# Optimization experiments

Hardware: AMD Instinct MI355X
Metric: run time of the kernel (lower is better)

## Reference

```python
import jax, jax.numpy as jnp
import numpy as np

H, F, E_SHARED, E_ROUTED, K = 1024, 4096, 1, 8, 2


def setup_inputs() -> dict:
    key = jax.random.key(0)
    ks = jax.random.split(key, 6)
    x = jax.random.normal(ks[0], (4, 2048, H), dtype=jnp.float32)
    s = 0.02
    shared_up = jax.random.normal(ks[1], (E_SHARED, H, F), dtype=jnp.float32) * s
    shared_down = jax.random.normal(ks[2], (E_SHARED, F, H), dtype=jnp.float32) * s
    routed_up = jax.random.normal(ks[3], (E_ROUTED, H, F), dtype=jnp.float32) * s
    routed_down = jax.random.normal(ks[4], (E_ROUTED, F, H), dtype=jnp.float32) * s
    router_w = jax.random.normal(ks[5], (H, E_ROUTED), dtype=jnp.float32) * s
    return {"x": x, "shared_up": shared_up, "shared_down": shared_down,
            "routed_up": routed_up, "routed_down": routed_down, "router_w": router_w}


def _expert(x, w_up, w_down):
    # ExpertBlock: down(gelu(up(x))), exact (erf) gelu as in torch F.gelu default
    h = jax.nn.gelu(jnp.einsum('bsh,hf->bsf', x, w_up), approximate=False)
    return jnp.einsum('bsf,fh->bsh', h, w_down)


def reference(x, shared_up, shared_down, routed_up, routed_down, router_w):
    # shared experts (always active)
    shared_out = jnp.zeros_like(x)
    for i in range(E_SHARED):
        shared_out = shared_out + _expert(x, shared_up[i], shared_down[i])

    # router: softmax over routed experts, then top-k gating
    probs = jax.nn.softmax(jnp.einsum('bsh,he->bse', x, router_w), axis=-1)
    top_k_prob, top_k_idx = jax.lax.top_k(probs, K)  # [B,S,K]
    # per-expert gate = sum of top-k probs assigned to that expert
    onehot = jax.nn.one_hot(top_k_idx, E_ROUTED, dtype=x.dtype)  # [B,S,K,E]
    gates = jnp.einsum('bsk,bske->bse', top_k_prob, onehot)      # [B,S,E]

    routed_out = jnp.zeros_like(x)
    for e in range(E_ROUTED):  # fixed small loop over experts
        y = _expert(x, routed_up[e], routed_down[e])
        routed_out = routed_out + gates[..., e:e + 1] * y

    return shared_out + routed_out + x
```

## Files before the change

kernel.cpp:

```cpp
#include <hip/hip_runtime.h>
#include <cstdint>
#include <cstddef>

#define HD 1024
#define FF 4096
#define TOK 8192
#define NSEG 9
#define ROWS_ROUTED (TOK*2)
#define ROWS_TOT (ROWS_ROUTED + TOK)

typedef __bf16 bf16;
typedef __bf16 bf16x8 __attribute__((ext_vector_type(8)));
typedef __bf16 bf16x4 __attribute__((ext_vector_type(4)));
typedef float  f32x4  __attribute__((ext_vector_type(4)));

__device__ __forceinline__ void stage16(const void* g, void* l) {
  __builtin_amdgcn_global_load_lds((const __attribute__((address_space(1))) void*)g,
                                   (__attribute__((address_space(3))) void*)l,
                                   16, 0, 0);
}

__device__ __forceinline__ unsigned short bf_bits(float v) {
  bf16 b = (bf16)v;
  return __builtin_bit_cast(unsigned short, b);
}

__device__ __forceinline__ int xcd_remap(int d) {
  return (((d >> 6) << 3) + (d & 7)) * 8 + ((d >> 3) & 7);
}

__global__ void k_init_meta(int* meta) {
  int t = threadIdx.x;
  if (t < 64) meta[t] = 0;
}

__global__ void k_convert_x(const float* __restrict__ x, bf16* __restrict__ xbf) {
  int i = blockIdx.x*256 + threadIdx.x;
  float4 v = reinterpret_cast<const float4*>(x)[i];
  ushort4 u;
  u.x = bf_bits(v.x); u.y = bf_bits(v.y); u.z = bf_bits(v.z); u.w = bf_bits(v.w);
  reinterpret_cast<ushort4*>(xbf)[i] = u;
}

__global__ void k_tcvt(const float* __restrict__ routed, const float* __restrict__ shared_,
                       bf16* __restrict__ dst, int R, int C) {
  int e = blockIdx.z;
  const float* src = (e < 8) ? (routed + (size_t)e*R*C) : shared_;
  bf16* d = dst + (size_t)e*R*C;
  __shared__ float lds[64][65];
  int r0 = blockIdx.y*64, c0 = blockIdx.x*64;
  int t = threadIdx.x;
  int tr = t>>4, tc4 = (t&15)*4;
  #pragma unroll
  for (int i=0;i<4;i++) {
    float4 v = *reinterpret_cast<const float4*>(src + (size_t)(r0+tr+i*16)*C + c0 + tc4);
    lds[tr+i*16][tc4+0]=v.x; lds[tr+i*16][tc4+1]=v.y;
    lds[tr+i*16][tc4+2]=v.z; lds[tr+i*16][tc4+3]=v.w;
  }
  __syncthreads();
  #pragma unroll
  for (int i=0;i<4;i++) {
    int oc = tr + i*16;
    ushort4 u;
    u.x = bf_bits(lds[tc4+0][oc]);
    u.y = bf_bits(lds[tc4+1][oc]);
    u.z = bf_bits(lds[tc4+2][oc]);
    u.w = bf_bits(lds[tc4+3][oc]);
    *reinterpret_cast<ushort4*>(d + (size_t)(c0+oc)*R + r0 + tc4) = u;
  }
}

__global__ void k_router(const float* __restrict__ x, const float* __restrict__ rw,
                         int* __restrict__ rtE, float* __restrict__ rtG,
                         int* __restrict__ meta) {
  __shared__ float rwl[HD*8];
  int t = threadIdx.x;
  for (int i=t;i<HD*8/4;i+=256)
    reinterpret_cast<float4*>(rwl)[i] = reinterpret_cast<const float4*>(rw)[i];
  __syncthreads();
  int wv = t>>6, lane = t&63;
  int tk = blockIdx.x*4 + wv;
  const float* xr = x + (size_t)tk*HD;
  float a[8] = {0,0,0,0,0,0,0,0};
  for (int i=0;i<HD/64;i++) {
    int h = lane + i*64;
    float xv = xr[h];
    const float* r = rwl + h*8;
    #pragma unroll
    for (int e=0;e<8;e++) a[e] = fmaf(xv, r[e], a[e]);
  }
  #pragma unroll
  for (int e=0;e<8;e++) {
    for (int s=32;s>0;s>>=1) a[e] += __shfl_xor(a[e], s, 64);
  }
  if (lane==0) {
    float mx = a[0];
    #pragma unroll
    for (int e=1;e<8;e++) mx = fmaxf(mx, a[e]);
    float p[8]; float den = 0.f;
    #pragma unroll
    for (int e=0;e<8;e++) { p[e] = expf(a[e]-mx); den += p[e]; }
    int i0 = 0;
    #pragma unroll
    for (int e=1;e<8;e++) if (p[e] > p[i0]) i0 = e;
    int i1 = (i0==0)?1:0;
    #pragma unroll
    for (int e=0;e<8;e++) if (e!=i0 && p[e] > p[i1]) i1 = e;
    float inv = 1.f/den;
    rtE[tk*2] = i0; rtE[tk*2+1] = i1;
    rtG[tk*2] = p[i0]*inv; rtG[tk*2+1] = p[i1]*inv;
    atomicAdd(&meta[i0], 1);
    atomicAdd(&meta[i1], 1);
  }
}

__global__ void k_prefix(int* meta) {
  if (threadIdx.x == 0) {
    int off = 0;
    for (int e=0;e<8;e++) { meta[16+e] = off; meta[32+e] = meta[e]; off += meta[e]; }
    meta[16+8] = ROWS_ROUTED;
    meta[32+8] = TOK;
  }
}

__global__ void k_scatter(const int* __restrict__ rtE, const float* __restrict__ rtG,
                          int* __restrict__ meta, int* __restrict__ tok,
                          float* __restrict__ gate, int* __restrict__ trow) {
  int t = blockIdx.x*256 + threadIdx.x;
  int e0 = rtE[t*2], e1 = rtE[t*2+1];
  float g0 = rtG[t*2], g1 = rtG[t*2+1];
  int p0 = atomicAdd(&meta[8+e0], 1);
  int r0 = meta[16+e0] + p0;
  tok[r0] = t; gate[r0] = g0; trow[t*2] = r0;
  int p1 = atomicAdd(&meta[8+e1], 1);
  int r1 = meta[16+e1] + p1;
  tok[r1] = t; gate[r1] = g1; trow[t*2+1] = r1;
  tok[ROWS_ROUTED + t] = t; gate[ROWS_ROUTED + t] = 1.0f;
}

__global__ void k_combine(const float* __restrict__ x, const bf16* __restrict__ dbuf,
                          const int* __restrict__ trow, float* __restrict__ out) {
  int tkn = blockIdx.x;
  int t = threadIdx.x;
  int r0 = trow[tkn*2], r1 = trow[tkn*2+1];
  int h = t*4;
  float4 xv = *reinterpret_cast<const float4*>(x + (size_t)tkn*HD + h);
  bf16x4 a = *reinterpret_cast<const bf16x4*>(dbuf + (size_t)(ROWS_ROUTED+tkn)*HD + h);
  bf16x4 b = *reinterpret_cast<const bf16x4*>(dbuf + (size_t)r0*HD + h);
  bf16x4 c = *reinterpret_cast<const bf16x4*>(dbuf + (size_t)r1*HD + h);
  float4 o;
  o.x = xv.x + (float)a[0] + (float)b[0] + (float)c[0];
  o.y = xv.y + (float)a[1] + (float)b[1] + (float)c[1];
  o.z = xv.z + (float)a[2] + (float)b[2] + (float)c[2];
  o.w = xv.w + (float)a[3] + (float)b[3] + (float)c[3];
  *reinterpret_cast<float4*>(out + (size_t)tkn*HD + h) = o;
}


__global__ __launch_bounds__(256,2) void k_gemm_up(
    const bf16* __restrict__ xbf, const bf16* __restrict__ wupT,
    bf16* __restrict__ hbuf, const int* __restrict__ tok,
    const int* __restrict__ meta)
{
  int bx = xcd_remap(blockIdx.x);
  int seg = bx >> 11;
  int rem = bx & 2047;
  int mt = rem >> 5, nt = rem & 31;
  int rows = (seg<8)? meta[32+seg] : TOK;
  if (mt*128 >= rows) return;
  int segoff = meta[16+seg];
  int rowbase = mt*128;

  __shared__ __align__(16) bf16 Alds[2][128*32];
  __shared__ __align__(16) bf16 Blds[2][128*32];

  const int t = threadIdx.x;
  const int lane = t & 63, w = t >> 6;

  int lr0 = t>>2, lr1 = 64 + (t>>2);
  int gr0 = rowbase + lr0; if (gr0 >= rows) gr0 = rowbase;
  int gr1 = rowbase + lr1; if (gr1 >= rows) gr1 = rowbase;
  int tok0 = tok[segoff + gr0], tok1 = tok[segoff + gr1];
  int kswz = ((t&3) ^ ((t>>3)&3)) * 8;
  const bf16* gA0 = xbf + (size_t)tok0*HD + kswz;
  const bf16* gA1 = xbf + (size_t)tok1*HD + kswz;
  const bf16* wb = wupT + (size_t)seg*FF*HD;
  int f0 = nt*128;
  const bf16* gB0 = wb + (size_t)(f0 + lr0)*HD + kswz;
  const bf16* gB1 = wb + (size_t)(f0 + lr1)*HD + kswz;

  char* AldsB = (char*)Alds; char* BldsB = (char*)Blds;
  const int stoff = w*1024;

  const int slotb = ((lane>>4) ^ (((lane&15)>>1)&3)) * 16;
  const int Afo = ((w>>1)*64 + (lane&15))*64 + slotb;
  const int Bfo = ((w&1)*64 + (lane&15))*64 + slotb;

  f32x4 acc[4][4] = {};

  stage16(gA0, AldsB + stoff);
  stage16(gA1, AldsB + 4096 + stoff);
  stage16(gB0, BldsB + stoff);
  stage16(gB1, BldsB + 4096 + stoff);
  __syncthreads();

  int cur = 0;
  for (int k0=32; k0<HD; k0+=32) {
    char* an = AldsB + (cur^1)*8192;
    char* bn = BldsB + (cur^1)*8192;
    stage16(gA0 + k0, an + stoff);
    stage16(gA1 + k0, an + 4096 + stoff);
    stage16(gB0 + k0, bn + stoff);
    stage16(gB1 + k0, bn + 4096 + stoff);
    const char* Ab = AldsB + cur*8192 + Afo;
    const char* Bb = BldsB + cur*8192 + Bfo;
    bf16x8 af[4], bfr[4];
    #pragma unroll
    for (int m=0;m<4;m++) af[m]  = *reinterpret_cast<const bf16x8*>(Ab + m*1024);
    #pragma unroll
    for (int n=0;n<4;n++) bfr[n] = *reinterpret_cast<const bf16x8*>(Bb + n*1024);
    #pragma unroll
    for (int m=0;m<4;m++)
      #pragma unroll
      for (int n=0;n<4;n++)
        acc[m][n] = __builtin_amdgcn_mfma_f32_16x16x32_bf16(bfr[n], af[m], acc[m][n], 0,0,0);
    __syncthreads();
    cur ^= 1;
  }
  {
    const char* Ab = AldsB + cur*8192 + Afo;
    const char* Bb = BldsB + cur*8192 + Bfo;
    bf16x8 af[4], bfr[4];
    #pragma unroll
    for (int m=0;m<4;m++) af[m]  = *reinterpret_cast<const bf16x8*>(Ab + m*1024);
    #pragma unroll
    for (int n=0;n<4;n++) bfr[n] = *reinterpret_cast<const bf16x8*>(Bb + n*1024);
    #pragma unroll
    for (int m=0;m<4;m++)
      #pragma unroll
      for (int n=0;n<4;n++)
        acc[m][n] = __builtin_amdgcn_mfma_f32_16x16x32_bf16(bfr[n], af[m], acc[m][n], 0,0,0);
  }

  const int lrm = lane&15, lq = lane>>4;
  #pragma unroll
  for (int m=0;m<4;m++) {
    int rl = (w>>1)*64 + m*16 + lrm;
    int gr = rowbase + rl;
    if (gr >= rows) continue;
    bf16* hrow = hbuf + (size_t)(segoff+gr)*FF + nt*128 + (w&1)*64 + lq*4;
    #pragma unroll
    for (int n=0;n<4;n++) {
      bf16x4 u;
      #pragma unroll
      for (int j=0;j<4;j++) {
        float v = acc[m][n][j];
        v = 0.5f*v*(1.0f + erff(v*0.70710678118654752f));
        u[j] = (bf16)v;
      }
      *reinterpret_cast<bf16x4*>(hrow + n*16) = u;
    }
  }
}

__global__ __launch_bounds__(256,2) void k_gemm_down(
    const bf16* __restrict__ hbuf, const bf16* __restrict__ wdnT,
    bf16* __restrict__ dbuf, const float* __restrict__ gate,
    const int* __restrict__ meta)
{
  int bx = xcd_remap(blockIdx.x);
  int seg = bx >> 9;
  int rem = bx & 511;
  int mt = rem >> 3, nt = rem & 7;
  int rows = (seg<8)? meta[32+seg] : TOK;
  if (mt*128 >= rows) return;
  int segoff = meta[16+seg];
  int rowbase = mt*128;

  __shared__ __align__(16) bf16 Alds[2][128*32];
  __shared__ __align__(16) bf16 Blds[2][128*32];
  __shared__ float gateL[128];

  const int t = threadIdx.x;
  const int lane = t & 63, w = t >> 6;

  if (t < 128) {
    int gr = rowbase + t; if (gr >= rows) gr = rows - 1;
    gateL[t] = gate[segoff + gr];
  }

  int lr0 = t>>2, lr1 = 64 + (t>>2);
  int kswz = ((t&3) ^ ((t>>3)&3)) * 8;
  const bf16* gA0 = hbuf + (size_t)(segoff + rowbase + lr0)*FF + kswz;
  const bf16* gA1 = hbuf + (size_t)(segoff + rowbase + lr1)*FF + kswz;
  const bf16* wb = wdnT + (size_t)seg*HD*FF;
  int h0 = nt*128;
  const bf16* gB0 = wb + (size_t)(h0 + lr0)*FF + kswz;
  const bf16* gB1 = wb + (size_t)(h0 + lr1)*FF + kswz;

  char* AldsB = (char*)Alds; char* BldsB = (char*)Blds;
  const int stoff = w*1024;

  const int slotb = ((lane>>4) ^ (((lane&15)>>1)&3)) * 16;
  const int Afo = ((w>>1)*64 + (lane&15))*64 + slotb;
  const int Bfo = ((w&1)*64 + (lane&15))*64 + slotb;

  f32x4 acc[4][4] = {};

  stage16(gA0, AldsB + stoff);
  stage16(gA1, AldsB + 4096 + stoff);
  stage16(gB0, BldsB + stoff);
  stage16(gB1, BldsB + 4096 + stoff);
  __syncthreads();

  int cur = 0;
  for (int k0=32; k0<FF; k0+=32) {
    char* an = AldsB + (cur^1)*8192;
    char* bn = BldsB + (cur^1)*8192;
    stage16(gA0 + k0, an + stoff);
    stage16(gA1 + k0, an + 4096 + stoff);
    stage16(gB0 + k0, bn + stoff);
    stage16(gB1 + k0, bn + 4096 + stoff);
    const char* Ab = AldsB + cur*8192 + Afo;
    const char* Bb = BldsB + cur*8192 + Bfo;
    bf16x8 af[4], bfr[4];
    #pragma unroll
    for (int m=0;m<4;m++) af[m]  = *reinterpret_cast<const bf16x8*>(Ab + m*1024);
    #pragma unroll
    for (int n=0;n<4;n++) bfr[n] = *reinterpret_cast<const bf16x8*>(Bb + n*1024);
    #pragma unroll
    for (int m=0;m<4;m++)
      #pragma unroll
      for (int n=0;n<4;n++)
        acc[m][n] = __builtin_amdgcn_mfma_f32_16x16x32_bf16(bfr[n], af[m], acc[m][n], 0,0,0);
    __syncthreads();
    cur ^= 1;
  }
  {
    const char* Ab = AldsB + cur*8192 + Afo;
    const char* Bb = BldsB + cur*8192 + Bfo;
    bf16x8 af[4], bfr[4];
    #pragma unroll
    for (int m=0;m<4;m++) af[m]  = *reinterpret_cast<const bf16x8*>(Ab + m*1024);
    #pragma unroll
    for (int n=0;n<4;n++) bfr[n] = *reinterpret_cast<const bf16x8*>(Bb + n*1024);
    #pragma unroll
    for (int m=0;m<4;m++)
      #pragma unroll
      for (int n=0;n<4;n++)
        acc[m][n] = __builtin_amdgcn_mfma_f32_16x16x32_bf16(bfr[n], af[m], acc[m][n], 0,0,0);
  }

  const int lrm = lane&15, lq = lane>>4;
  #pragma unroll
  for (int m=0;m<4;m++) {
    int rl = (w>>1)*64 + m*16 + lrm;
    int gr = rowbase + rl;
    if (gr >= rows) continue;
    float g = gateL[rl];
    bf16* drow = dbuf + (size_t)(segoff+gr)*HD + nt*128 + (w&1)*64 + lq*4;
    #pragma unroll
    for (int n=0;n<4;n++) {
      bf16x4 u;
      #pragma unroll
      for (int j=0;j<4;j++) u[j] = (bf16)(acc[m][n][j]*g);
      *reinterpret_cast<bf16x4*>(drow + n*16) = u;
    }
  }
}

struct Layout {
  size_t xbf, wupT, wdnT, hbuf, dbuf, tok, gate, trow, rtE, rtG, meta, total;
};

static inline Layout make_layout() {
  Layout L; size_t o = 0;
  auto al = [&](size_t b){ o = (o+255)&~(size_t)255; size_t r=o; o+=b; return r; };
  L.xbf  = al((size_t)TOK*HD*2);
  L.wupT = al((size_t)NSEG*FF*HD*2);
  L.wdnT = al((size_t)NSEG*FF*HD*2);
  L.hbuf = al((size_t)ROWS_TOT*FF*2);
  L.dbuf = al((size_t)ROWS_TOT*HD*2);
  L.tok  = al((size_t)ROWS_TOT*4);
  L.gate = al((size_t)ROWS_TOT*4);
  L.trow = al((size_t)TOK*2*4);
  L.rtE  = al((size_t)TOK*2*4);
  L.rtG  = al((size_t)TOK*2*4);
  L.meta = al(256*4);
  L.total = o;
  return L;
}

extern "C" void kernel_launch(void* const* d_in, const int* in_sizes, int n_in,
                              void* d_out, int out_size, void* d_ws, size_t ws_size,
                              hipStream_t stream) {
  const float* x           = (const float*)d_in[0];
  const float* shared_up   = (const float*)d_in[1];
  const float* shared_down = (const float*)d_in[2];
  const float* routed_up   = (const float*)d_in[3];
  const float* routed_down = (const float*)d_in[4];
  const float* router_w    = (const float*)d_in[5];
  float* out = (float*)d_out;

  Layout L = make_layout();
  char* ws = (char*)d_ws;
  bf16*  xbf  = (bf16*)(ws + L.xbf);
  bf16*  wupT = (bf16*)(ws + L.wupT);
  bf16*  wdnT = (bf16*)(ws + L.wdnT);
  bf16*  hbuf = (bf16*)(ws + L.hbuf);
  bf16*  dbuf = (bf16*)(ws + L.dbuf);
  int*   tok  = (int*)(ws + L.tok);
  float* gate = (float*)(ws + L.gate);
  int*   trow = (int*)(ws + L.trow);
  int*   rtE  = (int*)(ws + L.rtE);
  float* rtG  = (float*)(ws + L.rtG);
  int*   meta = (int*)(ws + L.meta);

  k_init_meta<<<1, 64, 0, stream>>>(meta);
  k_convert_x<<<TOK*HD/1024, 256, 0, stream>>>(x, xbf);
  k_tcvt<<<dim3(FF/64, HD/64, NSEG), 256, 0, stream>>>(routed_up, shared_up, wupT, HD, FF);
  k_tcvt<<<dim3(HD/64, FF/64, NSEG), 256, 0, stream>>>(routed_down, shared_down, wdnT, FF, HD);
  k_router<<<TOK/4, 256, 0, stream>>>(x, router_w, rtE, rtG, meta);
  k_prefix<<<1, 64, 0, stream>>>(meta);
  k_scatter<<<TOK/256, 256, 0, stream>>>(rtE, rtG, meta, tok, gate, trow);

  k_gemm_up<<<NSEG*64*32, 256, 0, stream>>>(xbf, wupT, hbuf, tok, meta);
  k_gemm_down<<<NSEG*64*8, 256, 0, stream>>>(hbuf, wdnT, dbuf, gate, meta);
  k_combine<<<TOK, 256, 0, stream>>>(x, dbuf, trow, out);
}
```

Baseline: 1.004 ms.

## Triple-buffer LDS staging with two-tile prefetch in expert GEMM kernels

```diff
diff --git a/kernel.cpp b/kernel.cpp
--- a/kernel.cpp
+++ b/kernel.cpp
@@ -157,7 +157,10 @@
 }
 
 
-__global__ __launch_bounds__(256,2) void k_gemm_up(
+#define NKU (HD/32)
+#define NKD (FF/32)
+
+__global__ __launch_bounds__(256,3) void k_gemm_up(
     const bf16* __restrict__ xbf, const bf16* __restrict__ wupT,
     bf16* __restrict__ hbuf, const int* __restrict__ tok,
     const int* __restrict__ meta)
@@ -171,8 +174,8 @@
   int segoff = meta[16+seg];
   int rowbase = mt*128;
 
-  __shared__ __align__(16) bf16 Alds[2][128*32];
-  __shared__ __align__(16) bf16 Blds[2][128*32];
+  __shared__ __align__(16) bf16 Alds[3][128*32];
+  __shared__ __align__(16) bf16 Blds[3][128*32];
 
   const int t = threadIdx.x;
   const int lane = t & 63, w = t >> 6;
@@ -198,20 +201,21 @@
 
   f32x4 acc[4][4] = {};
 
-  stage16(gA0, AldsB + stoff);
-  stage16(gA1, AldsB + 4096 + stoff);
-  stage16(gB0, BldsB + stoff);
-  stage16(gB1, BldsB + 4096 + stoff);
+  stage16(gA0,    AldsB + stoff); stage16(gA1,    AldsB + 4096 + stoff);
+  stage16(gB0,    BldsB + stoff); stage16(gB1,    BldsB + 4096 + stoff);
+  stage16(gA0+32, AldsB + 8192 + stoff); stage16(gA1+32, AldsB + 12288 + stoff);
+  stage16(gB0+32, BldsB + 8192 + stoff); stage16(gB1+32, BldsB + 12288 + stoff);
   __syncthreads();
 
   int cur = 0;
-  for (int k0=32; k0<HD; k0+=32) {
-    char* an = AldsB + (cur^1)*8192;
-    char* bn = BldsB + (cur^1)*8192;
-    stage16(gA0 + k0, an + stoff);
-    stage16(gA1 + k0, an + 4096 + stoff);
-    stage16(gB0 + k0, bn + stoff);
-    stage16(gB1 + k0, bn + 4096 + stoff);
+  for (int kt = 0; kt < NKU; ++kt) {
+    if (kt + 2 < NKU) {
+      int st = (cur >= 1) ? cur - 1 : 2;
+      int ko = (kt+2)*32;
+      char* an = AldsB + st*8192; char* bn = BldsB + st*8192;
+      stage16(gA0+ko, an + stoff); stage16(gA1+ko, an + 4096 + stoff);
+      stage16(gB0+ko, bn + stoff); stage16(gB1+ko, bn + 4096 + stoff);
+    }
     const char* Ab = AldsB + cur*8192 + Afo;
     const char* Bb = BldsB + cur*8192 + Bfo;
     bf16x8 af[4], bfr[4];
@@ -219,27 +223,17 @@
     for (int m=0;m<4;m++) af[m]  = *reinterpret_cast<const bf16x8*>(Ab + m*1024);
     #pragma unroll
     for (int n=0;n<4;n++) bfr[n] = *reinterpret_cast<const bf16x8*>(Bb + n*1024);
+    __builtin_amdgcn_s_setprio(1);
     #pragma unroll
     for (int m=0;m<4;m++)
       #pragma unroll
       for (int n=0;n<4;n++)
         acc[m][n] = __builtin_amdgcn_mfma_f32_16x16x32_bf16(bfr[n], af[m], acc[m][n], 0,0,0);
-    __syncthreads();
-    cur ^= 1;
-  }
-  {
-    const char* Ab = AldsB + cur*8192 + Afo;
-    const char* Bb = BldsB + cur*8192 + Bfo;
-    bf16x8 af[4], bfr[4];
-    #pragma unroll
-    for (int m=0;m<4;m++) af[m]  = *reinterpret_cast<const bf16x8*>(Ab + m*1024);
-    #pragma unroll
-    for (int n=0;n<4;n++) bfr[n] = *reinterpret_cast<const bf16x8*>(Bb + n*1024);
-    #pragma unroll
-    for (int m=0;m<4;m++)
-      #pragma unroll
-      for (int n=0;n<4;n++)
-        acc[m][n] = __builtin_amdgcn_mfma_f32_16x16x32_bf16(bfr[n], af[m], acc[m][n], 0,0,0);
+    __builtin_amdgcn_s_setprio(0);
+    if (kt + 2 < NKU)      asm volatile("s_waitcnt vmcnt(8)" ::: "memory");
+    else if (kt + 1 < NKU) asm volatile("s_waitcnt vmcnt(0)" ::: "memory");
+    if (kt + 1 < NKU) __builtin_amdgcn_s_barrier();
+    cur = (cur >= 2) ? 0 : cur + 1;
   }
 
   const int lrm = lane&15, lq = lane>>4;
@@ -263,7 +257,7 @@
   }
 }
 
-__global__ __launch_bounds__(256,2) void k_gemm_down(
+__global__ __launch_bounds__(256,3) void k_gemm_down(
     const bf16* __restrict__ hbuf, const bf16* __restrict__ wdnT,
     bf16* __restrict__ dbuf, const float* __restrict__ gate,
     const int* __restrict__ meta)
@@ -277,8 +271,8 @@
   int segoff = meta[16+seg];
   int rowbase = mt*128;
 
-  __shared__ __align__(16) bf16 Alds[2][128*32];
-  __shared__ __align__(16) bf16 Blds[2][128*32];
+  __shared__ __align__(16) bf16 Alds[3][128*32];
+  __shared__ __align__(16) bf16 Blds[3][128*32];
   __shared__ float gateL[128];
 
   const int t = threadIdx.x;
@@ -307,20 +301,21 @@
 
   f32x4 acc[4][4] = {};
 
-  stage16(gA0, AldsB + stoff);
-  stage16(gA1, AldsB + 4096 + stoff);
-  stage16(gB0, BldsB + stoff);
-  stage16(gB1, BldsB + 4096 + stoff);
+  stage16(gA0,    AldsB + stoff); stage16(gA1,    AldsB + 4096 + stoff);
+  stage16(gB0,    BldsB + stoff); stage16(gB1,    BldsB + 4096 + stoff);
+  stage16(gA0+32, AldsB + 8192 + stoff); stage16(gA1+32, AldsB + 12288 + stoff);
+  stage16(gB0+32, BldsB + 8192 + stoff); stage16(gB1+32, BldsB + 12288 + stoff);
   __syncthreads();
 
   int cur = 0;
-  for (int k0=32; k0<FF; k0+=32) {
-    char* an = AldsB + (cur^1)*8192;
-    char* bn = BldsB + (cur^1)*8192;
-    stage16(gA0 + k0, an + stoff);
-    stage16(gA1 + k0, an + 4096 + stoff);
-    stage16(gB0 + k0, bn + stoff);
-    stage16(gB1 + k0, bn + 4096 + stoff);
+  for (int kt = 0; kt < NKD; ++kt) {
+    if (kt + 2 < NKD) {
+      int st = (cur >= 1) ? cur - 1 : 2;
+      int ko = (kt+2)*32;
+      char* an = AldsB + st*8192; char* bn = BldsB + st*8192;
+      stage16(gA0+ko, an + stoff); stage16(gA1+ko, an + 4096 + stoff);
+      stage16(gB0+ko, bn + stoff); stage16(gB1+ko, bn + 4096 + stoff);
+    }
     const char* Ab = AldsB + cur*8192 + Afo;
     const char* Bb = BldsB + cur*8192 + Bfo;
     bf16x8 af[4], bfr[4];
@@ -328,27 +323,17 @@
     for (int m=0;m<4;m++) af[m]  = *reinterpret_cast<const bf16x8*>(Ab + m*1024);
     #pragma unroll
     for (int n=0;n<4;n++) bfr[n] = *reinterpret_cast<const bf16x8*>(Bb + n*1024);
+    __builtin_amdgcn_s_setprio(1);
     #pragma unroll
     for (int m=0;m<4;m++)
       #pragma unroll
       for (int n=0;n<4;n++)
         acc[m][n] = __builtin_amdgcn_mfma_f32_16x16x32_bf16(bfr[n], af[m], acc[m][n], 0,0,0);
-    __syncthreads();
-    cur ^= 1;
-  }
-  {
-    const char* Ab = AldsB + cur*8192 + Afo;
-    const char* Bb = BldsB + cur*8192 + Bfo;
-    bf16x8 af[4], bfr[4];
-    #pragma unroll
-    for (int m=0;m<4;m++) af[m]  = *reinterpret_cast<const bf16x8*>(Ab + m*1024);
-    #pragma unroll
-    for (int n=0;n<4;n++) bfr[n] = *reinterpret_cast<const bf16x8*>(Bb + n*1024);
-    #pragma unroll
-    for (int m=0;m<4;m++)
-      #pragma unroll
-      for (int n=0;n<4;n++)
-        acc[m][n] = __builtin_amdgcn_mfma_f32_16x16x32_bf16(bfr[n], af[m], acc[m][n], 0,0,0);
+    __builtin_amdgcn_s_setprio(0);
+    if (kt + 2 < NKD)      asm volatile("s_waitcnt vmcnt(8)" ::: "memory");
+    else if (kt + 1 < NKD) asm volatile("s_waitcnt vmcnt(0)" ::: "memory");
+    if (kt + 1 < NKD) __builtin_amdgcn_s_barrier();
+    cur = (cur >= 2) ? 0 : cur + 1;
   }
 
   const int lrm = lane&15, lq = lane>>4;
```

After: 1.046 ms. 1.04x slower.
